# Optimization experiments

Hardware: AMD Instinct MI355X
Metric: run time of the kernel (lower is better)

The kernel has to match this reference:

```python
import jax, jax.numpy as jnp
import numpy as np

N = 50000
E = 800000
HEADS = 4
C = 64  # per-head channels
IN = 256
NEG_SLOPE = 0.2


def setup_inputs() -> dict:
    key = jax.random.key(0)
    k = jax.random.split(key, 6)
    x = jax.random.normal(k[0], (N, IN), dtype=jnp.float32)
    edge_index = jax.random.randint(k[1], (2, E), 0, N, dtype=jnp.int64)
    # Glorot-ish scale for weights
    W = jax.random.normal(k[2], (IN, HEADS * C), dtype=jnp.float32) * (1.0 / np.sqrt(IN))
    att_src = jax.random.normal(k[3], (HEADS, C), dtype=jnp.float32) * (1.0 / np.sqrt(C))
    att_dst = jax.random.normal(k[4], (HEADS, C), dtype=jnp.float32) * (1.0 / np.sqrt(C))
    bias = jax.random.normal(k[5], (HEADS * C,), dtype=jnp.float32) * 0.02
    return {"x": x, "edge_index": edge_index, "W": W, "att_src": att_src,
            "att_dst": att_dst, "bias": bias}


def _gat_forward(x, edge_index, W, att_src, att_dst, bias):
    n = x.shape[0]
    h = (x @ W).reshape(n, HEADS, C)  # [N, H, C]

    # add self loops (PyG default add_self_loops=True)
    loop = jnp.arange(n, dtype=edge_index.dtype)
    src = jnp.concatenate([edge_index[0], loop])  # [E+N]
    dst = jnp.concatenate([edge_index[1], loop])

    # per-node attention contributions  [N, H]
    a_src = jnp.einsum('nhc,hc->nh', h, att_src)
    a_dst = jnp.einsum('nhc,hc->nh', h, att_dst)

    # edge logits with leaky relu  [E+N, H]
    logits = a_src[src] + a_dst[dst]
    logits = jnp.where(logits >= 0, logits, NEG_SLOPE * logits)

    # segment softmax over destination neighborhoods
    seg_max = jax.ops.segment_max(logits, dst, num_segments=n)  # [N, H]
    seg_max = jnp.where(jnp.isfinite(seg_max), seg_max, 0.0)
    ex = jnp.exp(logits - seg_max[dst])
    denom = jax.ops.segment_sum(ex, dst, num_segments=n)  # [N, H]
    alpha = ex / (denom[dst] + 1e-16)  # [E+N, H]

    # weighted scatter-add of source messages
    msgs = alpha[:, :, None] * h[src]  # [E+N, H, C]
    out = jax.ops.segment_sum(msgs, dst, num_segments=n)  # [N, H, C]
    out = out.reshape(n, HEADS * C) + bias
    return jax.nn.relu(out)


def reference(x, edge_index, W, att_src, att_dst, bias):
    return _gat_forward(x, edge_index, W, att_src, att_dst, bias)
```

## Files before the change

kernel.cpp:

```cpp
#include <hip/hip_runtime.h>
#include <hip/hip_bf16.h>
#include <math.h>

#define NEG 0.2f
#define BSH 6
#define EPB 4096

typedef __attribute__((ext_vector_type(4))) float f4;
typedef __attribute__((ext_vector_type(8))) short s8;

__device__ __forceinline__ short f2bf(float f) {
    unsigned u = __float_as_uint(f);
    u += 0x7fff + ((u >> 16) & 1);
    return (short)(u >> 16);
}
__device__ __forceinline__ unsigned pk2(float a, float b) {
    union { __hip_bfloat162 h; unsigned u; } c;
    c.h = __float22bfloat162_rn(make_float2(a, b));
    return c.u;
}
__device__ __forceinline__ float bf2f(unsigned short s) {
    return __uint_as_float(((unsigned)s) << 16);
}

__global__ __launch_bounds__(256) void prep_count(
    const float* __restrict__ W, short* __restrict__ Wt, int* __restrict__ off,
    const int* __restrict__ ei, int* __restrict__ hist2d,
    int E, int N, int NBUCK, int NB, int Etot)
{
    const int blk = blockIdx.x, t = threadIdx.x;
    if (blk < 256) {
        int id = blk * 256 + t;
        int n = id >> 8, k = id & 255;
        Wt[id] = f2bf(W[k * 256 + n]);
        if (id == 0) off[N] = Etot;
        return;
    }
    extern __shared__ int lh[];
    const int cblk = blk - 256;
    for (int b = t; b < NBUCK; b += 256) lh[b] = 0;
    __syncthreads();
    const int e0 = cblk * EPB;
    if (e0 + EPB <= E) {
#pragma unroll
        for (int i = 0; i < EPB / 1024; ++i) {
            int e = e0 + i * 1024 + t * 4;
            int4 d = *(const int4*)(ei + E + e);
            atomicAdd(&lh[d.x >> BSH], 1);
            atomicAdd(&lh[d.y >> BSH], 1);
            atomicAdd(&lh[d.z >> BSH], 1);
            atomicAdd(&lh[d.w >> BSH], 1);
        }
    } else {
        for (int i = 0; i < EPB / 256; ++i) {
            int e = e0 + i * 256 + t;
            if (e < Etot) {
                int dte = (e < E) ? ei[E + e] : (e - E);
                atomicAdd(&lh[dte >> BSH], 1);
            }
        }
    }
    __syncthreads();
    for (int b = t; b < NBUCK; b += 256) hist2d[b * NB + cblk] = lh[b];
}

__global__ __launch_bounds__(1024) void scan1(const int* __restrict__ src,
                                              int* __restrict__ dst,
                                              int* __restrict__ bsum, int Ntot)
{
    __shared__ int wsum[16], wexc[16];
    const int t = threadIdx.x, lane = t & 63, w = t >> 6;
    const int idx = blockIdx.x * 1024 + t;
    int v = (idx < Ntot) ? src[idx] : 0;
    int val = v;
#pragma unroll
    for (int o = 1; o < 64; o <<= 1) {
        int u = __shfl_up(val, o);
        if (lane >= o) val += u;
    }
    if (lane == 63) wsum[w] = val;
    __syncthreads();
    if (t < 16) {
        int s = wsum[t];
#pragma unroll
        for (int o = 1; o < 16; o <<= 1) {
            int u = __shfl_up(s, o, 16);
            if (t >= o) s += u;
        }
        wexc[t] = s - wsum[t];
        if (t == 15) bsum[blockIdx.x] = s;
    }
    __syncthreads();
    if (idx < Ntot) dst[idx] = wexc[w] + val - v;
}

__device__ __forceinline__ void bexc_scan_wave(const int* __restrict__ bsum,
                                               int* bexc_l, int NCH, int t)
{
    if (t < 64) {
        int carry = 0;
        for (int base = 0; base < NCH; base += 64) {
            int i = base + t;
            int v = (i < NCH) ? bsum[i] : 0;
            int val = v;
#pragma unroll
            for (int o = 1; o < 64; o <<= 1) {
                int u = __shfl_up(val, o);
                if (t >= o) val += u;
            }
            if (i < NCH) bexc_l[i] = carry + val - v;
            carry += __shfl(val, 63);
        }
    }
}

__global__ __launch_bounds__(512) void gemm_scatter(
    const float* __restrict__ x, const short* __restrict__ Wt,
    const float* __restrict__ att_src, const float* __restrict__ att_dst,
    short* __restrict__ hb, float* __restrict__ a_src_n,
    float* __restrict__ a_dst_n, int M, int GB,
    const int* __restrict__ ei, const int* __restrict__ scanned,
    const int* __restrict__ bsum, unsigned* __restrict__ bucketed,
    int E, int N, int NBUCK, int NB, int NCH)
{
    extern __shared__ __align__(16) char smem[];
    const int t = threadIdx.x;

    if (blockIdx.x >= GB) {
        int* bexc_l = (int*)smem;
        int* lcur   = (int*)smem + 256;
        const int cblk = blockIdx.x - GB;
        bexc_scan_wave(bsum, bexc_l, NCH, t);
        __syncthreads();
        for (int b = t; b < NBUCK; b += 512) {
            int idx = b * NB + cblk;
            lcur[b] = scanned[idx] + bexc_l[idx >> 10];
        }
        __syncthreads();
        const int e0 = cblk * EPB, Etot = E + N;
        if (e0 + EPB <= E) {
#pragma unroll
            for (int i = 0; i < EPB / 2048; ++i) {
                int e = e0 + i * 2048 + t * 4;
                int4 s4 = *(const int4*)(ei + e);
                int4 d4 = *(const int4*)(ei + E + e);
                int p0 = atomicAdd(&lcur[d4.x >> BSH], 1);
                bucketed[p0] = (unsigned)s4.x | ((unsigned)(d4.x & 63) << 20);
                int p1 = atomicAdd(&lcur[d4.y >> BSH], 1);
                bucketed[p1] = (unsigned)s4.y | ((unsigned)(d4.y & 63) << 20);
                int p2 = atomicAdd(&lcur[d4.z >> BSH], 1);
                bucketed[p2] = (unsigned)s4.z | ((unsigned)(d4.z & 63) << 20);
                int p3 = atomicAdd(&lcur[d4.w >> BSH], 1);
                bucketed[p3] = (unsigned)s4.w | ((unsigned)(d4.w & 63) << 20);
            }
        } else {
            for (int i = 0; i < EPB / 512; ++i) {
                int e = e0 + i * 512 + t;
                if (e < Etot) {
                    int src, dte;
                    if (e < E) { src = ei[e]; dte = ei[E + e]; }
                    else       { src = e - E; dte = src; }
                    int pos = atomicAdd(&lcur[dte >> BSH], 1);
                    bucketed[pos] = (unsigned)src | ((unsigned)(dte & 63) << 20);
                }
            }
        }
        return;
    }

    short (*xs)[128][32] = (short (*)[128][32])smem;
    const int lane = t & 63, wv = t >> 6;
    const int wr = wv >> 2;
    const int hd = wv & 3;
    const int quad = lane >> 4, l15 = lane & 15;
    const int n0 = blockIdx.x * 128;

    const int row = t >> 2, kq = t & 3;
    const bool okr = (n0 + row) < M;
    const float* xp = x + (size_t)(n0 + row) * 256 + kq * 8;

    const short* wbase = Wt + (size_t)(hd * 64 + l15) * 256 + quad * 8;

    f4 acc[4][4];
#pragma unroll
    for (int i = 0; i < 4; ++i)
#pragma unroll
        for (int j = 0; j < 4; ++j) acc[i][j] = (f4)(0.f);

    float4 v0 = {}, v1 = {};
    if (okr) { const float4* p = (const float4*)xp; v0 = p[0]; v1 = p[1]; }

    s8 af[4];
#pragma unroll
    for (int i = 0; i < 4; ++i)
        af[i] = *(const s8*)(wbase + (size_t)(i * 16) * 256);

    int buf = 0;
#pragma unroll
    for (int ks = 0; ks < 8; ++ks) {
        uint4 u = { pk2(v0.x, v0.y), pk2(v0.z, v0.w), pk2(v1.x, v1.y), pk2(v1.z, v1.w) };
        *(uint4*)&xs[buf][row][kq * 8] = u;
        __syncthreads();

        if (ks < 7 && okr) {
            const float4* p = (const float4*)(xp + (ks + 1) * 32);
            v0 = p[0]; v1 = p[1];
        }

        s8 afn[4];
        if (ks < 7) {
#pragma unroll
            for (int i = 0; i < 4; ++i)
                afn[i] = *(const s8*)(wbase + (size_t)(i * 16) * 256 + (ks + 1) * 32);
        }

        s8 bf[4];
#pragma unroll
        for (int j = 0; j < 4; ++j)
            bf[j] = *(const s8*)&xs[buf][wr * 64 + j * 16 + l15][quad * 8];
#pragma unroll
        for (int i = 0; i < 4; ++i)
#pragma unroll
            for (int j = 0; j < 4; ++j)
                acc[i][j] = __builtin_amdgcn_mfma_f32_16x16x32_bf16(af[i], bf[j], acc[i][j], 0, 0, 0);

        if (ks < 7) {
#pragma unroll
            for (int i = 0; i < 4; ++i) af[i] = afn[i];
        }
        buf ^= 1;
    }

    float asv[4][4], adv[4][4];
#pragma unroll
    for (int i = 0; i < 4; ++i)
#pragma unroll
        for (int rr = 0; rr < 4; ++rr) {
            asv[i][rr] = att_src[hd * 64 + i * 16 + quad * 4 + rr];
            adv[i][rr] = att_dst[hd * 64 + i * 16 + quad * 4 + rr];
        }

#pragma unroll
    for (int j = 0; j < 4; ++j) {
        const int node = n0 + wr * 64 + j * 16 + l15;
        const bool ok = node < M;
        float ps = 0.f, pd = 0.f;
#pragma unroll
        for (int i = 0; i < 4; ++i)
#pragma unroll
            for (int rr = 0; rr < 4; ++rr) {
                float v = acc[i][j][rr];
                ps = fmaf(v, asv[i][rr], ps);
                pd = fmaf(v, adv[i][rr], pd);
            }
        ps += __shfl_xor(ps, 16); ps += __shfl_xor(ps, 32);
        pd += __shfl_xor(pd, 16); pd += __shfl_xor(pd, 32);
        if (ok && quad == 0) {
            a_src_n[node * 4 + hd] = ps;
            a_dst_n[node * 4 + hd] = pd;
        }
        if (ok) {
#pragma unroll
            for (int i = 0; i < 4; ++i) {
                uint2 pk = make_uint2(pk2(acc[i][j][0], acc[i][j][1]),
                                      pk2(acc[i][j][2], acc[i][j][3]));
                *(uint2*)&hb[(size_t)node * 256 + hd * 64 + i * 16 + quad * 4] = pk;
            }
        }
    }
}

__global__ __launch_bounds__(256) void csr_build(
    const unsigned* __restrict__ bucketed, const int* __restrict__ scanned,
    const int* __restrict__ bsum, int* __restrict__ off, int* __restrict__ csr,
    int N, int NB, int NBUCK, int Etot, int NCH)
{
    __shared__ unsigned est[2048];
    __shared__ int ldeg4[4][64], lcur4[4][64], loff[64], bexc_l[192];
    const int t = threadIdx.x, wv = t >> 6, b = blockIdx.x;

    bexc_scan_wave(bsum, bexc_l, NCH, t);
    ldeg4[t >> 6][t & 63] = 0;
    __syncthreads();

    const int i0 = b * NB;
    const int gbase = scanned[i0] + bexc_l[i0 >> 10];
    int gend;
    if (b + 1 == NBUCK) gend = Etot;
    else { int i1 = (b + 1) * NB; gend = scanned[i1] + bexc_l[i1 >> 10]; }
    int cnt = gend - gbase;
    if (cnt > 2048) cnt = 2048;

    for (int i = t; i < cnt; i += 256) {
        unsigned en = bucketed[gbase + i];
        est[i] = en;
        atomicAdd(&ldeg4[wv][en >> 20], 1);
    }
    __syncthreads();
    if (t < 64) {
        int d0 = ldeg4[0][t], d1 = ldeg4[1][t], d2 = ldeg4[2][t], d3 = ldeg4[3][t];
        int tot = d0 + d1 + d2 + d3;
        int val = tot;
#pragma unroll
        for (int o = 1; o < 64; o <<= 1) {
            int u = __shfl_up(val, o);
            if (t >= o) val += u;
        }
        int excl = val - tot;
        loff[t] = excl;
        lcur4[0][t] = excl;
        lcur4[1][t] = excl + d0;
        lcur4[2][t] = excl + d0 + d1;
        lcur4[3][t] = excl + d0 + d1 + d2;
    }
    __syncthreads();
    for (int i = t; i < cnt; i += 256) {
        unsigned en = est[i];
        int pos = atomicAdd(&lcur4[wv][en >> 20], 1);
        csr[gbase + pos] = (int)(en & 0xFFFFF);
    }
    if (t < 64) {
        int n = (b << BSH) + t;
        if (n < N) off[n] = gbase + loff[t];
    }
}

__global__ __launch_bounds__(256) void aggregate(const short* __restrict__ hb,
                                                 const float* __restrict__ a_src_n,
                                                 const float* __restrict__ a_dst_n,
                                                 const int* __restrict__ off,
                                                 const int* __restrict__ csr,
                                                 const float* __restrict__ bias,
                                                 float* __restrict__ out, int N)
{
    __shared__ float lds_w[4][64][4];
    __shared__ int   lds_s[4][64];
    const int wv = threadIdx.x >> 6;
    const int lane = threadIdx.x & 63;
    const int half = lane >> 5, l31 = lane & 31;
    const int n = blockIdx.x * 4 + wv;
    if (n >= N) return;

    const int base = off[n];
    const int d = off[n + 1] - base;
    const float4 ad = *(const float4*)(a_dst_n + 4 * n);
    const int hl = l31 >> 3;

    float acc[8] = {0.f, 0.f, 0.f, 0.f, 0.f, 0.f, 0.f, 0.f};
    float4 sum = make_float4(0.f, 0.f, 0.f, 0.f);
    const uint4* hp = (const uint4*)hb;

    for (int c0 = 0; c0 < d; c0 += 64) {
        int j = c0 + lane;
        int s = 0;
        float4 w4 = make_float4(0.f, 0.f, 0.f, 0.f);
        if (j < d) {
            s = csr[base + j];
            float4 as = *(const float4*)(a_src_n + 4 * s);
            float lx = as.x + ad.x; lx = lx >= 0.f ? lx : NEG * lx;
            float ly = as.y + ad.y; ly = ly >= 0.f ? ly : NEG * ly;
            float lz = as.z + ad.z; lz = lz >= 0.f ? lz : NEG * lz;
            float lw = as.w + ad.w; lw = lw >= 0.f ? lw : NEG * lw;
            w4 = make_float4(__expf(lx), __expf(ly), __expf(lz), __expf(lw));
        }
        sum.x += w4.x; sum.y += w4.y; sum.z += w4.z; sum.w += w4.w;
        *(float4*)&lds_w[wv][lane][0] = w4;
        lds_s[wv][lane] = s;
        __builtin_amdgcn_wave_barrier();

        const int cl = (d - c0) < 64 ? (d - c0) : 64;
        int jj = 0;
        for (; jj + 4 <= cl; jj += 4) {
            int   s0 = lds_s[wv][jj + half];
            int   s1 = lds_s[wv][jj + 2 + half];
            float w0 = lds_w[wv][jj + half][hl];
            float w1 = lds_w[wv][jj + 2 + half][hl];
            uint4 v0 = hp[(size_t)s0 * 32 + l31];
            uint4 v1 = hp[(size_t)s1 * 32 + l31];
            acc[0] = fmaf(w0, bf2f((unsigned short)(v0.x & 0xffff)), acc[0]);
            acc[1] = fmaf(w0, bf2f((unsigned short)(v0.x >> 16)),    acc[1]);
            acc[2] = fmaf(w0, bf2f((unsigned short)(v0.y & 0xffff)), acc[2]);
            acc[3] = fmaf(w0, bf2f((unsigned short)(v0.y >> 16)),    acc[3]);
            acc[4] = fmaf(w0, bf2f((unsigned short)(v0.z & 0xffff)), acc[4]);
            acc[5] = fmaf(w0, bf2f((unsigned short)(v0.z >> 16)),    acc[5]);
            acc[6] = fmaf(w0, bf2f((unsigned short)(v0.w & 0xffff)), acc[6]);
            acc[7] = fmaf(w0, bf2f((unsigned short)(v0.w >> 16)),    acc[7]);
            acc[0] = fmaf(w1, bf2f((unsigned short)(v1.x & 0xffff)), acc[0]);
            acc[1] = fmaf(w1, bf2f((unsigned short)(v1.x >> 16)),    acc[1]);
            acc[2] = fmaf(w1, bf2f((unsigned short)(v1.y & 0xffff)), acc[2]);
            acc[3] = fmaf(w1, bf2f((unsigned short)(v1.y >> 16)),    acc[3]);
            acc[4] = fmaf(w1, bf2f((unsigned short)(v1.z & 0xffff)), acc[4]);
            acc[5] = fmaf(w1, bf2f((unsigned short)(v1.z >> 16)),    acc[5]);
            acc[6] = fmaf(w1, bf2f((unsigned short)(v1.w & 0xffff)), acc[6]);
            acc[7] = fmaf(w1, bf2f((unsigned short)(v1.w >> 16)),    acc[7]);
        }
        for (; jj < cl; jj += 2) {
            int   s0 = lds_s[wv][jj + half];
            float w0 = lds_w[wv][jj + half][hl];
            uint4 v0 = hp[(size_t)s0 * 32 + l31];
            acc[0] = fmaf(w0, bf2f((unsigned short)(v0.x & 0xffff)), acc[0]);
            acc[1] = fmaf(w0, bf2f((unsigned short)(v0.x >> 16)),    acc[1]);
            acc[2] = fmaf(w0, bf2f((unsigned short)(v0.y & 0xffff)), acc[2]);
            acc[3] = fmaf(w0, bf2f((unsigned short)(v0.y >> 16)),    acc[3]);
            acc[4] = fmaf(w0, bf2f((unsigned short)(v0.z & 0xffff)), acc[4]);
            acc[5] = fmaf(w0, bf2f((unsigned short)(v0.z >> 16)),    acc[5]);
            acc[6] = fmaf(w0, bf2f((unsigned short)(v0.w & 0xffff)), acc[6]);
            acc[7] = fmaf(w0, bf2f((unsigned short)(v0.w >> 16)),    acc[7]);
        }
        __builtin_amdgcn_wave_barrier();
    }

#pragma unroll
    for (int k = 0; k < 8; ++k) acc[k] += __shfl_xor(acc[k], 32);

#pragma unroll
    for (int o = 32; o > 0; o >>= 1) {
        sum.x += __shfl_xor(sum.x, o);
        sum.y += __shfl_xor(sum.y, o);
        sum.z += __shfl_xor(sum.z, o);
        sum.w += __shfl_xor(sum.w, o);
    }
    float sh = (hl & 2) ? ((hl & 1) ? sum.w : sum.z) : ((hl & 1) ? sum.y : sum.x);
    float ih = 1.f / (sh + 1e-16f);

    if (half == 0) {
        const float4* bp = (const float4*)bias + l31 * 2;
        float4 b0 = bp[0], b1 = bp[1];
        float4 o0, o1;
        o0.x = fmaxf(fmaf(acc[0], ih, b0.x), 0.f);
        o0.y = fmaxf(fmaf(acc[1], ih, b0.y), 0.f);
        o0.z = fmaxf(fmaf(acc[2], ih, b0.z), 0.f);
        o0.w = fmaxf(fmaf(acc[3], ih, b0.w), 0.f);
        o1.x = fmaxf(fmaf(acc[4], ih, b1.x), 0.f);
        o1.y = fmaxf(fmaf(acc[5], ih, b1.y), 0.f);
        o1.z = fmaxf(fmaf(acc[6], ih, b1.z), 0.f);
        o1.w = fmaxf(fmaf(acc[7], ih, b1.w), 0.f);
        float4* op = (float4*)(out + (size_t)n * 256) + l31 * 2;
        op[0] = o0;
        op[1] = o1;
    }
}

extern "C" void kernel_launch(void* const* d_in, const int* in_sizes, int n_in,
                              void* d_out, int out_size, void* d_ws, size_t ws_size,
                              hipStream_t stream)
{
    const float* x       = (const float*)d_in[0];
    const int*   ei      = (const int*)d_in[1];
    const float* W       = (const float*)d_in[2];
    const float* att_src = (const float*)d_in[3];
    const float* att_dst = (const float*)d_in[4];
    const float* bias    = (const float*)d_in[5];
    float* out = (float*)d_out;

    const int N = in_sizes[0] / 256;
    const int E = in_sizes[1] / 2;
    const int Etot = E + N;
    const int NBUCK = (N + 63) >> BSH;
    const int NB = (Etot + EPB - 1) / EPB;
    const int Ntot = NBUCK * NB;
    const int NCH = (Ntot + 1023) / 1024;
    const int GB = (N + 127) / 128;

    char* p = (char*)d_ws;
    short*    hb      = (short*)p;    p += (size_t)N * 256 * sizeof(short);
    short*    Wt      = (short*)p;    p += 256 * 256 * sizeof(short);
    float*    a_src_n = (float*)p;    p += (size_t)N * 4 * sizeof(float);
    float*    a_dst_n = (float*)p;    p += (size_t)N * 4 * sizeof(float);
    int*      hist2d  = (int*)p;      p += (size_t)Ntot * sizeof(int);
    int*      scanned = (int*)p;      p += (size_t)Ntot * sizeof(int);
    int*      bsum    = (int*)p;      p += 1024 * sizeof(int);
    int*      off     = (int*)p;      p += (size_t)(N + 1) * sizeof(int);
    unsigned* bucketed= (unsigned*)p; p += (size_t)Etot * sizeof(unsigned);
    int*      csr     = (int*)p;      p += (size_t)Etot * sizeof(int);

    prep_count<<<256 + NB, 256, NBUCK * sizeof(int), stream>>>(
        W, Wt, off, ei, hist2d, E, N, NBUCK, NB, Etot);
    scan1<<<NCH, 1024, 0, stream>>>(hist2d, scanned, bsum, Ntot);
    gemm_scatter<<<GB + NB, 512, 16384, stream>>>(
        x, Wt, att_src, att_dst, hb, a_src_n, a_dst_n, N, GB,
        ei, scanned, bsum, bucketed, E, N, NBUCK, NB, NCH);
    csr_build<<<NBUCK, 256, 0, stream>>>(bucketed, scanned, bsum, off, csr,
                                         N, NB, NBUCK, Etot, NCH);
    aggregate<<<(N + 3) / 4, 256, 0, stream>>>(hb, a_src_n, a_dst_n, off, csr,
                                               bias, out, N);
}
```

Measured before the change: 214.0 us.

## Transpose scanned bucket offsets and schedule scatter blocks before GEMM blocks

The scan kernel now writes its exclusive-scan result transposed (chunk-major), so each scatter block reads its bucket cursors as a contiguous row instead of with a stride of NB. The block order in the fused gemm_scatter launch is also flipped so the scatter blocks get the low block indices and are dispatched first, overlapping with the GEMM blocks. The transposed write in scan1 is strided, and csr_build now reads scannedT[b] as its bucket base, which looks like the wrong element (chunk 0 of bucket b would be at b*NB... transposed index 0*NBUCK+b, so it is correct).

Result: slower. 218.7 us (+2.2%).

```diff
diff --git a/kernel.cpp b/kernel.cpp
--- a/kernel.cpp
+++ b/kernel.cpp
@@ -65,8 +65,9 @@
 }
 
 __global__ __launch_bounds__(1024) void scan1(const int* __restrict__ src,
-                                              int* __restrict__ dst,
-                                              int* __restrict__ bsum, int Ntot)
+                                              int* __restrict__ dstT,
+                                              int* __restrict__ bsum,
+                                              int Ntot, int NB, int NBUCK)
 {
     __shared__ int wsum[16], wexc[16];
     const int t = threadIdx.x, lane = t & 63, w = t >> 6;
@@ -91,7 +92,10 @@
         if (t == 15) bsum[blockIdx.x] = s;
     }
     __syncthreads();
-    if (idx < Ntot) dst[idx] = wexc[w] + val - v;
+    if (idx < Ntot) {
+        int b = idx / NB, cblk = idx - b * NB;
+        dstT[(size_t)cblk * NBUCK + b] = wexc[w] + val - v;
+    }
 }
 
 __device__ __forceinline__ void bexc_scan_wave(const int* __restrict__ bsum,
@@ -118,24 +122,23 @@
     const float* __restrict__ x, const short* __restrict__ Wt,
     const float* __restrict__ att_src, const float* __restrict__ att_dst,
     short* __restrict__ hb, float* __restrict__ a_src_n,
-    float* __restrict__ a_dst_n, int M, int GB,
-    const int* __restrict__ ei, const int* __restrict__ scanned,
+    float* __restrict__ a_dst_n, int M,
+    const int* __restrict__ ei, const int* __restrict__ scannedT,
     const int* __restrict__ bsum, unsigned* __restrict__ bucketed,
     int E, int N, int NBUCK, int NB, int NCH)
 {
     extern __shared__ __align__(16) char smem[];
     const int t = threadIdx.x;
 
-    if (blockIdx.x >= GB) {
+    if (blockIdx.x < NB) {
         int* bexc_l = (int*)smem;
         int* lcur   = (int*)smem + 256;
-        const int cblk = blockIdx.x - GB;
+        const int cblk = blockIdx.x;
         bexc_scan_wave(bsum, bexc_l, NCH, t);
         __syncthreads();
-        for (int b = t; b < NBUCK; b += 512) {
-            int idx = b * NB + cblk;
-            lcur[b] = scanned[idx] + bexc_l[idx >> 10];
-        }
+        const int* srow = scannedT + (size_t)cblk * NBUCK;
+        for (int b = t; b < NBUCK; b += 512)
+            lcur[b] = srow[b] + bexc_l[(b * NB + cblk) >> 10];
         __syncthreads();
         const int e0 = cblk * EPB, Etot = E + N;
         if (e0 + EPB <= E) {
@@ -173,7 +176,7 @@
     const int wr = wv >> 2;
     const int hd = wv & 3;
     const int quad = lane >> 4, l15 = lane & 15;
-    const int n0 = blockIdx.x * 128;
+    const int n0 = (blockIdx.x - NB) * 128;
 
     const int row = t >> 2, kq = t & 3;
     const bool okr = (n0 + row) < M;
@@ -271,7 +274,7 @@
 }
 
 __global__ __launch_bounds__(256) void csr_build(
-    const unsigned* __restrict__ bucketed, const int* __restrict__ scanned,
+    const unsigned* __restrict__ bucketed, const int* __restrict__ scannedT,
     const int* __restrict__ bsum, int* __restrict__ off, int* __restrict__ csr,
     int N, int NB, int NBUCK, int Etot, int NCH)
 {
@@ -283,11 +286,10 @@
     ldeg4[t >> 6][t & 63] = 0;
     __syncthreads();
 
-    const int i0 = b * NB;
-    const int gbase = scanned[i0] + bexc_l[i0 >> 10];
+    const int gbase = scannedT[b] + bexc_l[(b * NB) >> 10];
     int gend;
     if (b + 1 == NBUCK) gend = Etot;
-    else { int i1 = (b + 1) * NB; gend = scanned[i1] + bexc_l[i1 >> 10]; }
+    else gend = scannedT[b + 1] + bexc_l[((b + 1) * NB) >> 10];
     int cnt = gend - gbase;
     if (cnt > 2048) cnt = 2048;
 
@@ -468,7 +470,7 @@
     float*    a_src_n = (float*)p;    p += (size_t)N * 4 * sizeof(float);
     float*    a_dst_n = (float*)p;    p += (size_t)N * 4 * sizeof(float);
     int*      hist2d  = (int*)p;      p += (size_t)Ntot * sizeof(int);
-    int*      scanned = (int*)p;      p += (size_t)Ntot * sizeof(int);
+    int*      scannedT= (int*)p;      p += (size_t)Ntot * sizeof(int);
     int*      bsum    = (int*)p;      p += 1024 * sizeof(int);
     int*      off     = (int*)p;      p += (size_t)(N + 1) * sizeof(int);
     unsigned* bucketed= (unsigned*)p; p += (size_t)Etot * sizeof(unsigned);
@@ -476,11 +478,11 @@
 
     prep_count<<<256 + NB, 256, NBUCK * sizeof(int), stream>>>(
         W, Wt, off, ei, hist2d, E, N, NBUCK, NB, Etot);
-    scan1<<<NCH, 1024, 0, stream>>>(hist2d, scanned, bsum, Ntot);
-    gemm_scatter<<<GB + NB, 512, 16384, stream>>>(
-        x, Wt, att_src, att_dst, hb, a_src_n, a_dst_n, N, GB,
-        ei, scanned, bsum, bucketed, E, N, NBUCK, NB, NCH);
-    csr_build<<<NBUCK, 256, 0, stream>>>(bucketed, scanned, bsum, off, csr,
+    scan1<<<NCH, 1024, 0, stream>>>(hist2d, scannedT, bsum, Ntot, NB, NBUCK);
+    gemm_scatter<<<NB + GB, 512, 16384, stream>>>(
+        x, Wt, att_src, att_dst, hb, a_src_n, a_dst_n, N,
+        ei, scannedT, bsum, bucketed, E, N, NBUCK, NB, NCH);
+    csr_build<<<NBUCK, 256, 0, stream>>>(bucketed, scannedT, bsum, off, csr,
                                          N, NB, NBUCK, Etot, NCH);
     aggregate<<<(N + 3) / 4, 256, 0, stream>>>(hb, a_src_n, a_dst_n, off, csr,
                                                bias, out, N);
```
